# Kernel optimization log

Hardware: AMD Instinct MI355X
Metric: run time of the kernel (lower is better)

The kernel has to match this reference:

```python
import jax, jax.numpy as jnp
import numpy as np

D_MODEL = 1024
NUM_HEADS = 16
DEPTH = D_MODEL // NUM_HEADS
B, S = 2, 2048


def setup_inputs() -> dict:
    key = jax.random.key(0)
    ks = jax.random.split(key, 12)
    scale = 1.0 / np.sqrt(D_MODEL)
    inp = {
        'q': jax.random.normal(ks[0], (B, S, D_MODEL), dtype=jnp.float32),
        'k': jax.random.normal(ks[1], (B, S, D_MODEL), dtype=jnp.float32),
        'v': jax.random.normal(ks[2], (B, S, D_MODEL), dtype=jnp.float32),
        'mask': jnp.zeros((1, 1, S, S), dtype=jnp.float32),
        'wq': jax.random.normal(ks[3], (D_MODEL, D_MODEL), dtype=jnp.float32) * scale,
        'bq': jnp.zeros((D_MODEL,), dtype=jnp.float32),
        'wk': jax.random.normal(ks[4], (D_MODEL, D_MODEL), dtype=jnp.float32) * scale,
        'bk': jnp.zeros((D_MODEL,), dtype=jnp.float32),
        'wv': jax.random.normal(ks[5], (D_MODEL, D_MODEL), dtype=jnp.float32) * scale,
        'bv': jnp.zeros((D_MODEL,), dtype=jnp.float32),
        'wo': jax.random.normal(ks[6], (D_MODEL, D_MODEL), dtype=jnp.float32) * scale,
        'bo': jnp.zeros((D_MODEL,), dtype=jnp.float32),
    }
    return inp


def _split_heads(x):
    # [B, S, D] -> [B, H, S, depth]
    b, s, _ = x.shape
    return x.reshape(b, s, NUM_HEADS, DEPTH).transpose(0, 2, 1, 3)


def reference(q, k, v, mask, wq, bq, wk, bk, wv, bv, wo, bo):
    qh = _split_heads(q @ wq + bq)   # [B,H,S,depth]
    kh = _split_heads(k @ wk + bk)
    vh = _split_heads(v @ wv + bv)
    logits = jnp.einsum('bhqd,bhkd->bhqk', qh, kh) / jnp.sqrt(jnp.float32(DEPTH))
    logits = logits + mask * (-1e9)
    attn = jax.nn.softmax(logits, axis=-1)
    out = jnp.einsum('bhqk,bhkd->bhqd', attn, vh)  # [B,H,S,depth]
    out = out.transpose(0, 2, 1, 3).reshape(q.shape[0], -1, D_MODEL)
    return out @ wo + bo
```

## Files before the change

### kernel.cpp

```cpp
#include <hip/hip_runtime.h>

typedef unsigned short u16;
typedef unsigned int   u32;
typedef unsigned long long u64;
typedef short s16;

using f32x4  = __attribute__((ext_vector_type(4))) float;
using bf16x8 = __attribute__((ext_vector_type(8))) __bf16;
using bf16x4 = __attribute__((ext_vector_type(4))) __bf16;
using u16x8  = __attribute__((ext_vector_type(8))) u16;
using u16x4  = __attribute__((ext_vector_type(4))) u16;
using s16x4  = __attribute__((ext_vector_type(4))) s16;

#define LOG2E 1.4426950408889634f

__device__ __forceinline__ u16 f2bf(float f) {
  u32 u = __builtin_bit_cast(u32, f);
  u32 r = u + 0x7fffu + ((u >> 16) & 1u);
  return (u16)(r >> 16);
}

__device__ __forceinline__ float ex2(float x) {
#if __has_builtin(__builtin_amdgcn_exp2f)
  return __builtin_amdgcn_exp2f(x);
#else
  return exp2f(x);
#endif
}

__device__ __forceinline__ u16x4 pack4(float p0, float p1, float p2, float p3) {
  bf16x4 b = {(__bf16)p0, (__bf16)p1, (__bf16)p2, (__bf16)p3};
  return __builtin_bit_cast(u16x4, b);
}

__device__ __forceinline__ void gll16(const u16* g, u16* l) {
  __builtin_amdgcn_global_load_lds(
      (const __attribute__((address_space(1))) void*)g,
      (__attribute__((address_space(3))) void*)l, 16, 0, 0);
}

__device__ __forceinline__ bf16x8 ld_bf8(const u16* p) {
  return __builtin_bit_cast(bf16x8, *(const u16x8*)p);
}

__device__ __forceinline__ bf16x8 cat8(u16x4 a, u16x4 b) {
  u16x8 r = {a[0], a[1], a[2], a[3], b[0], b[1], b[2], b[3]};
  return __builtin_bit_cast(bf16x8, r);
}

__device__ __forceinline__ f32x4 mfma32(bf16x8 a, bf16x8 b, f32x4 c) {
  return __builtin_amdgcn_mfma_f32_16x16x32_bf16(a, b, c, 0, 0, 0);
}

__device__ __forceinline__ int swz_r(int g) { return g >> 2; }
__device__ __forceinline__ int swz_c(int g) { return (g & 3) ^ ((g >> 3) & 3); }
__device__ __forceinline__ int swz_off(int r, int c) {
  return (r * 4 + (c ^ ((r >> 1) & 3))) * 8;
}

__global__ __launch_bounds__(256) void pre_kernel(
    const float* __restrict__ q, const float* __restrict__ k,
    const float* __restrict__ v, const float* __restrict__ mask,
    const float* __restrict__ wq, const float* __restrict__ wk,
    const float* __restrict__ wv, const float* __restrict__ wo,
    u16* __restrict__ qb, u16* __restrict__ kb, u16* __restrict__ vb,
    u16* __restrict__ wqT, u16* __restrict__ wkT, u16* __restrict__ wvT,
    u16* __restrict__ woT, int* flag) {
  int y = blockIdx.y, t = threadIdx.x;
  if (y < 3) {
    const float* src = y == 0 ? q : y == 1 ? k : v;
    u16* dst = y == 0 ? qb : y == 1 ? kb : vb;
    u64 i = ((u64)blockIdx.x * 256 + t) * 8;
    f32x4 a = *(const f32x4*)(src + i);
    f32x4 b = *(const f32x4*)(src + i + 4);
    u16x8 o;
    o[0] = f2bf(a[0]); o[1] = f2bf(a[1]); o[2] = f2bf(a[2]); o[3] = f2bf(a[3]);
    o[4] = f2bf(b[0]); o[5] = f2bf(b[1]); o[6] = f2bf(b[2]); o[7] = f2bf(b[3]);
    *(u16x8*)(dst + i) = o;
  } else if (y == 3) {
    __shared__ float tile[32][33];
    int x = t & 31, yy = t >> 5;
#pragma unroll
    for (int rep = 0; rep < 2; ++rep) {
      int job = blockIdx.x * 2 + rep;
      int z = job >> 10, tt = job & 1023;
      const float* W = z == 0 ? wq : z == 1 ? wk : z == 2 ? wv : wo;
      u16* WT = z == 0 ? wqT : z == 1 ? wkT : z == 2 ? wvT : woT;
      int c0 = (tt & 31) * 32, r0 = (tt >> 5) * 32;
#pragma unroll
      for (int j = 0; j < 4; ++j)
        tile[yy + j * 8][x] = W[(u64)(r0 + yy + j * 8) * 1024 + c0 + x];
      __syncthreads();
#pragma unroll
      for (int j = 0; j < 4; ++j)
        WT[(u64)(c0 + yy + j * 8) * 1024 + r0 + x] = f2bf(tile[x][yy + j * 8]);
      __syncthreads();
    }
  } else {
    u64 i = ((u64)blockIdx.x * 256 + t) * 8;
    f32x4 a = *(const f32x4*)(mask + i);
    f32x4 b = *(const f32x4*)(mask + i + 4);
    bool nz = a[0] != 0.f || a[1] != 0.f || a[2] != 0.f || a[3] != 0.f ||
              b[0] != 0.f || b[1] != 0.f || b[2] != 0.f || b[3] != 0.f;
    if (nz) atomicOr(flag, 1);
  }
}

__device__ __forceinline__ void gemm_core(const u16* __restrict__ A,
                                          const u16* __restrict__ Wt, int m0,
                                          int n0, u16* SH, f32x4 acc[4][4]) {
  int t = threadIdx.x, w = t >> 6, lane = t & 63;
  int quad = lane >> 4, l16 = lane & 15;
  int wr = w >> 1, wc = w & 1;
  const u16* a0 = A + (u64)(m0 + swz_r(t)) * 1024 + swz_c(t) * 8;
  const u16* a1 = A + (u64)(m0 + swz_r(256 + t)) * 1024 + swz_c(256 + t) * 8;
  const u16* bg0 = Wt + (u64)(n0 + swz_r(t)) * 1024 + swz_c(t) * 8;
  const u16* bg1 = Wt + (u64)(n0 + swz_r(256 + t)) * 1024 + swz_c(256 + t) * 8;
  int aoff[4], boff[4];
#pragma unroll
  for (int i = 0; i < 4; ++i) {
    aoff[i] = swz_off(wr * 64 + i * 16 + l16, quad);
    boff[i] = 4096 + swz_off(wc * 64 + i * 16 + l16, quad);
  }
#define QSTAGE(buf, kt)                                         \
  gll16(a0 + (kt), &SH[(buf) * 8192 + t * 8]);                  \
  gll16(bg0 + (kt), &SH[(buf) * 8192 + 4096 + t * 8]);          \
  gll16(a1 + (kt), &SH[(buf) * 8192 + (256 + t) * 8]);          \
  gll16(bg1 + (kt), &SH[(buf) * 8192 + 4096 + (256 + t) * 8]);
  QSTAGE(0, 0);
  asm volatile("s_waitcnt vmcnt(0)" ::: "memory");
  __builtin_amdgcn_s_barrier();
  __builtin_amdgcn_sched_barrier(0);
#pragma unroll
  for (int T = 0; T < 32; ++T) {
    if (T + 1 < 32) { QSTAGE((T + 1) & 1, (T + 1) * 32); }
    const u16* S = SH + (T & 1) * 8192;
    bf16x8 af[4], bfr[4];
#pragma unroll
    for (int i = 0; i < 4; ++i) af[i] = ld_bf8(&S[aoff[i]]);
#pragma unroll
    for (int i = 0; i < 4; ++i) bfr[i] = ld_bf8(&S[boff[i]]);
#pragma unroll
    for (int mi = 0; mi < 4; ++mi)
#pragma unroll
      for (int ni = 0; ni < 4; ++ni)
        acc[mi][ni] = mfma32(af[mi], bfr[ni], acc[mi][ni]);
    asm volatile("s_waitcnt vmcnt(0)" ::: "memory");
    __builtin_amdgcn_s_barrier();
    __builtin_amdgcn_sched_barrier(0);
  }
#undef QSTAGE
}

__global__ __launch_bounds__(256, 3) void qkv_gemm(
    const u16* __restrict__ qb, const u16* __restrict__ kb,
    const u16* __restrict__ vb, const u16* __restrict__ wqT,
    const u16* __restrict__ wkT, const u16* __restrict__ wvT,
    const float* __restrict__ bq, const float* __restrict__ bk,
    const float* __restrict__ bv, u16* __restrict__ Qh,
    u16* __restrict__ Khs, u16* __restrict__ Vhs) {
  int z = blockIdx.z;
  const u16* A = z == 0 ? qb : z == 1 ? kb : vb;
  const u16* Wt = z == 0 ? wqT : z == 1 ? wkT : wvT;
  const float* bias = z == 0 ? bq : z == 1 ? bk : bv;
  int m0 = blockIdx.x * 128, n0 = blockIdx.y * 128;
  __shared__ __align__(16) u16 SH[18432];
  f32x4 acc[4][4] = {};
  gemm_core(A, Wt, m0, n0, SH, acc);
  int t = threadIdx.x, w = t >> 6, lane = t & 63;
  int quad = lane >> 4, l16 = lane & 15;
  int wr = w >> 1, wc = w & 1;
  int h = (n0 + wc * 64) >> 6;
  if (z == 2) {
#pragma unroll
    for (int mi = 0; mi < 4; ++mi) {
      int gm0 = m0 + wr * 64 + mi * 16;
      int bh = (gm0 >> 11) * 16 + h;
      int tIdx = (gm0 & 2047) >> 6;
      int kvq = ((gm0 & 63) >> 2) + quad;
      u16* tile = Vhs + ((u64)(bh * 32 + tIdx)) * 4096;
#pragma unroll
      for (int ni = 0; ni < 4; ++ni) {
        int d = ni * 16 + l16;
        float bv_ = bias[n0 + wc * 64 + d];
        u16x4 pv = pack4(acc[mi][ni][0] + bv_, acc[mi][ni][1] + bv_,
                         acc[mi][ni][2] + bv_, acc[mi][ni][3] + bv_);
        *(u16x4*)&tile[(kvq * 64 + d) * 4] = pv;
      }
    }
  } else {
    __syncthreads();
    u16* TB = SH + w * 2304;
    float scale = (z == 0) ? (LOG2E / 8.f) : 1.f;
#pragma unroll
    for (int p = 0; p < 2; ++p) {
#pragma unroll
      for (int mi2 = 0; mi2 < 2; ++mi2)
#pragma unroll
        for (int ni = 0; ni < 4; ++ni) {
          int d = ni * 16 + l16;
          float bv_ = bias[n0 + wc * 64 + d];
#pragma unroll
          for (int r = 0; r < 4; ++r) {
            int kvloc = mi2 * 16 + quad * 4 + r;
            TB[kvloc * 72 + d] =
                f2bf((acc[p * 2 + mi2][ni][r] + bv_) * scale);
          }
        }
      int gm0 = m0 + wr * 64 + p * 32;
      int bh = (gm0 >> 11) * 16 + h;
#pragma unroll
      for (int i = 0; i < 4; ++i) {
        int g = i * 64 + lane;
        int kvloc = g >> 3, slot = g & 7;
        if (z == 0) {
          u16x8 gran = *(u16x8*)&TB[kvloc * 72 + slot * 8];
          int s = (gm0 & 2047) + kvloc;
          *(u16x8*)&Qh[((u64)bh * 2048 + s) * 64 + slot * 8] = gran;
        } else {
          int kk = (kvloc & 3) | ((kvloc >> 1) & 4);
          u16x8 gran = *(u16x8*)&TB[kvloc * 72 + (slot ^ kk) * 8];
          int tIdx = (gm0 & 2047) >> 6;
          int kv = (gm0 & 63) + kvloc;
          *(u16x8*)&Khs[((u64)(bh * 32 + tIdx)) * 4096 + kv * 64 + slot * 8] =
              gran;
        }
      }
    }
  }
}

template <int CUR>
__device__ __forceinline__ void fa_fast_step(
    int T, int t, int quad, int l16, int x7,
    const u16* __restrict__ Kg0, const u16* __restrict__ Vg0, u16* Kb0,
    u16* Vb0, bf16x8 aq0, bf16x8 aq1, f32x4 (&o)[4], f32x4& l_acc,
    bf16x8 ones8) {
  if (T + 1 < 32) {
    gll16(Kg0 + (u64)(T + 1) * 4096 + t * 8, &Kb0[(CUR ^ 1) * 4096 + t * 8]);
    gll16(Vg0 + (u64)(T + 1) * 4096 + t * 8, &Vb0[(CUR ^ 1) * 4096 + t * 8]);
  }
  const u16* Kt = Kb0 + CUR * 4096;
  const u16* Vt = Vb0 + CUR * 4096;
  int lbase = (l16 >> 2) * 8 + (l16 & 3);
  u16x4 pk[4];
#pragma unroll
  for (int cc = 0; cc < 4; ++cc) {
    int kvr = (cc >> 1) * 32 + (cc & 1) * 4 + lbase;
    bf16x8 k0 = ld_bf8(&Kt[kvr * 64 + ((quad ^ x7)) * 8]);
    bf16x8 k1 = ld_bf8(&Kt[kvr * 64 + (((quad + 4) ^ x7)) * 8]);
    f32x4 s_ = {};
    s_ = mfma32(k0, aq0, s_);
    s_ = mfma32(k1, aq1, s_);
    pk[cc] = pack4(ex2(s_[0]), ex2(s_[1]), ex2(s_[2]), ex2(s_[3]));
  }
  __builtin_amdgcn_s_setprio(1);
#pragma unroll
  for (int g = 0; g < 2; ++g) {
    bf16x8 pa = cat8(pk[g * 2], pk[g * 2 + 1]);
    l_acc = mfma32(pa, ones8, l_acc);
#pragma unroll
    for (int nt = 0; nt < 4; ++nt) {
      const u16* vb = &Vt[(((g * 8 + quad * 2) * 64) + nt * 16 + l16) * 4];
      bf16x8 vf = cat8(*(const u16x4*)vb, *(const u16x4*)(vb + 256));
      o[nt] = mfma32(pa, vf, o[nt]);
    }
  }
  __builtin_amdgcn_s_setprio(0);
  __syncthreads();
}

template <int CUR>
__device__ __forceinline__ void fa_mask_step(
    int T, int t, int lane, int quad, int l16, int x7, int qg,
    const u16* __restrict__ Kg0, const u16* __restrict__ Vg0,
    const float* __restrict__ mask, u16* Kb0, u16* Vb0, bf16x8 aq0,
    bf16x8 aq1, f32x4 (&o)[4], float& m_r, float& l_r) {
  if (T + 1 < 32) {
    gll16(Kg0 + (u64)(T + 1) * 4096 + t * 8, &Kb0[(CUR ^ 1) * 4096 + t * 8]);
    gll16(Vg0 + (u64)(T + 1) * 4096 + t * 8, &Vb0[(CUR ^ 1) * 4096 + t * 8]);
  }
  const u16* Kt = Kb0 + CUR * 4096;
  const u16* Vt = Vb0 + CUR * 4096;
  int lbase = (l16 >> 2) * 8 + (l16 & 3);
  f32x4 sv[4];
#pragma unroll
  for (int cc = 0; cc < 4; ++cc) {
    int kvr = (cc >> 1) * 32 + (cc & 1) * 4 + lbase;
    bf16x8 k0 = ld_bf8(&Kt[kvr * 64 + ((quad ^ x7)) * 8]);
    bf16x8 k1 = ld_bf8(&Kt[kvr * 64 + (((quad + 4) ^ x7)) * 8]);
    f32x4 s_ = {};
    s_ = mfma32(k0, aq0, s_);
    s_ = mfma32(k1, aq1, s_);
    sv[cc] = s_;
  }
#pragma unroll
  for (int cc = 0; cc < 4; ++cc)
#pragma unroll
    for (int r = 0; r < 4; ++r)
      sv[cc][r] += mask[(u64)qg * 2048 + T * 64 + (cc >> 1) * 32 + quad * 8 +
                        (cc & 1) * 4 + r] *
                   (-1e9f * LOG2E);
  float mx = -1e30f;
#pragma unroll
  for (int cc = 0; cc < 4; ++cc)
    mx = fmaxf(mx, fmaxf(fmaxf(sv[cc][0], sv[cc][1]),
                         fmaxf(sv[cc][2], sv[cc][3])));
  mx = fmaxf(mx, __shfl_xor(mx, 16));
  mx = fmaxf(mx, __shfl_xor(mx, 32));
  float mnew = fmaxf(m_r, mx);
  float alpha = ex2(m_r - mnew);
  m_r = mnew;
  float rs = 0.f;
  u16x4 pk[4];
#pragma unroll
  for (int cc = 0; cc < 4; ++cc) {
    float p0 = ex2(sv[cc][0] - m_r), p1 = ex2(sv[cc][1] - m_r);
    float p2 = ex2(sv[cc][2] - m_r), p3 = ex2(sv[cc][3] - m_r);
    rs += (p0 + p1) + (p2 + p3);
    pk[cc] = pack4(p0, p1, p2, p3);
  }
  rs += __shfl_xor(rs, 16);
  rs += __shfl_xor(rs, 32);
  l_r = l_r * alpha + rs;
  float a4[4];
#pragma unroll
  for (int r = 0; r < 4; ++r)
    a4[r] = __shfl(alpha, (lane & 48) | (quad * 4 + r));
#pragma unroll
  for (int nt = 0; nt < 4; ++nt)
#pragma unroll
    for (int r = 0; r < 4; ++r) o[nt][r] *= a4[r];
  __builtin_amdgcn_s_setprio(1);
#pragma unroll
  for (int g = 0; g < 2; ++g) {
    bf16x8 pa = cat8(pk[g * 2], pk[g * 2 + 1]);
#pragma unroll
    for (int nt = 0; nt < 4; ++nt) {
      const u16* vb = &Vt[(((g * 8 + quad * 2) * 64) + nt * 16 + l16) * 4];
      bf16x8 vf = cat8(*(const u16x4*)vb, *(const u16x4*)(vb + 256));
      o[nt] = mfma32(pa, vf, o[nt]);
    }
  }
  __builtin_amdgcn_s_setprio(0);
  __syncthreads();
}

__global__ __launch_bounds__(512, 4) void flash_attn(
    const u16* __restrict__ Qh, const u16* __restrict__ Khs,
    const u16* __restrict__ Vhs, const float* __restrict__ mask,
    const int* __restrict__ flag, u16* __restrict__ Ob) {
  int L = blockIdx.x + (blockIdx.y << 4);
  int bh = (L & 7) * 4 + ((L >> 3) & 3);
  int q0 = (L >> 5) * 128;
  int t = threadIdx.x, w = t >> 6, lane = t & 63;
  int quad = lane >> 4, l16 = lane & 15;
  __shared__ u16 SMEM[16384];
  u16* Kb0 = SMEM;
  u16* Vb0 = SMEM + 8192;
  const u16* Kg0 = Khs + (u64)bh * 32 * 4096;
  const u16* Vg0 = Vhs + (u64)bh * 32 * 4096;
  const u16* Qbase = Qh + ((u64)bh * 2048 + q0 + w * 16 + l16) * 64 + quad * 8;
  bf16x8 aq0 = ld_bf8(Qbase);
  bf16x8 aq1 = ld_bf8(Qbase + 32);
  f32x4 o[4] = {};
  const bool use_mask = (*flag) != 0;
  int x7 = l16 & 7;
  const u16x8 ones8u = {0x3F80, 0x3F80, 0x3F80, 0x3F80,
                        0x3F80, 0x3F80, 0x3F80, 0x3F80};
  bf16x8 ones8 = __builtin_bit_cast(bf16x8, ones8u);
  gll16(Kg0 + t * 8, &Kb0[t * 8]);
  gll16(Vg0 + t * 8, &Vb0[t * 8]);
  __syncthreads();
  int b = bh >> 4, h = bh & 15;
  if (!use_mask) {
    f32x4 l_acc = {};
    for (int T = 0; T < 32; T += 2) {
      fa_fast_step<0>(T, t, quad, l16, x7, Kg0, Vg0, Kb0, Vb0, aq0, aq1, o,
                      l_acc, ones8);
      fa_fast_step<1>(T + 1, t, quad, l16, x7, Kg0, Vg0, Kb0, Vb0, aq0, aq1,
                      o, l_acc, ones8);
    }
    float rl[4];
#pragma unroll
    for (int r = 0; r < 4; ++r) rl[r] = 1.f / l_acc[r];
#pragma unroll
    for (int nt = 0; nt < 4; ++nt)
#pragma unroll
      for (int r = 0; r < 4; ++r) {
        int srow = q0 + w * 16 + quad * 4 + r;
        Ob[(u64)(b * 2048 + srow) * 1024 + h * 64 + nt * 16 + l16] =
            f2bf(o[nt][r] * rl[r]);
      }
  } else {
    float m_r = -1e30f, l_r = 0.f;
    int qg = q0 + w * 16 + l16;
    for (int T = 0; T < 32; T += 2) {
      fa_mask_step<0>(T, t, lane, quad, l16, x7, qg, Kg0, Vg0, mask, Kb0, Vb0,
                      aq0, aq1, o, m_r, l_r);
      fa_mask_step<1>(T + 1, t, lane, quad, l16, x7, qg, Kg0, Vg0, mask, Kb0,
                      Vb0, aq0, aq1, o, m_r, l_r);
    }
    float rl[4];
#pragma unroll
    for (int r = 0; r < 4; ++r)
      rl[r] = 1.f / __shfl(l_r, (lane & 48) | (quad * 4 + r));
#pragma unroll
    for (int nt = 0; nt < 4; ++nt)
#pragma unroll
      for (int r = 0; r < 4; ++r) {
        int srow = q0 + w * 16 + quad * 4 + r;
        Ob[(u64)(b * 2048 + srow) * 1024 + h * 64 + nt * 16 + l16] =
            f2bf(o[nt][r] * rl[r]);
      }
  }
}

__global__ __launch_bounds__(256, 2) void out_gemm(const u16* __restrict__ Ob,
                                                   const u16* __restrict__ woT,
                                                   const float* __restrict__ bo,
                                                   float* __restrict__ out) {
  int m0 = blockIdx.x * 128, n0 = blockIdx.y * 64;
  __shared__ __align__(16) u16 SH[24576];
  f32x4 acc[2][4] = {};
  int t = threadIdx.x, w = t >> 6, lane = t & 63;
  int quad = lane >> 4, l16 = lane & 15;
  const u16* ag[4];
  const u16* bgp[2];
#pragma unroll
  for (int j = 0; j < 4; ++j) {
    int g = j * 256 + t, row = g >> 3, cc = (g & 7) ^ (row & 7);
    ag[j] = Ob + (u64)(m0 + row) * 1024 + cc * 8;
  }
#pragma unroll
  for (int j = 0; j < 2; ++j) {
    int g = j * 256 + t, row = g >> 3, cc = (g & 7) ^ (row & 7);
    bgp[j] = woT + (u64)(n0 + row) * 1024 + cc * 8;
  }
#define OSTAGE(buf, kt)                                              \
  {                                                                  \
    u16* D = &SH[(buf) * 12288];                                     \
    gll16(ag[0] + (kt), &D[t * 8]);                                  \
    gll16(ag[1] + (kt), &D[(256 + t) * 8]);                          \
    gll16(ag[2] + (kt), &D[(512 + t) * 8]);                          \
    gll16(ag[3] + (kt), &D[(768 + t) * 8]);                          \
    gll16(bgp[0] + (kt), &D[8192 + t * 8]);                          \
    gll16(bgp[1] + (kt), &D[8192 + (256 + t) * 8]);                  \
  }
  OSTAGE(0, 0);
  asm volatile("s_waitcnt vmcnt(0)" ::: "memory");
  __builtin_amdgcn_s_barrier();
  __builtin_amdgcn_sched_barrier(0);
#pragma unroll
  for (int T = 0; T < 16; ++T) {
    if (T + 1 < 16) { OSTAGE((T + 1) & 1, (T + 1) * 64); }
    const u16* S = SH + (T & 1) * 12288;
#pragma unroll
    for (int ks = 0; ks < 2; ++ks) {
      bf16x8 af[2], bfr[4];
#pragma unroll
      for (int i = 0; i < 2; ++i) {
        int r = w * 32 + i * 16 + l16;
        af[i] = ld_bf8(&S[(r * 8 + ((ks * 4 + quad) ^ (r & 7))) * 8]);
      }
#pragma unroll
      for (int i = 0; i < 4; ++i) {
        int r = i * 16 + l16;
        bfr[i] = ld_bf8(&S[8192 + (r * 8 + ((ks * 4 + quad) ^ (r & 7))) * 8]);
      }
#pragma unroll
      for (int mi = 0; mi < 2; ++mi)
#pragma unroll
        for (int ni = 0; ni < 4; ++ni)
          acc[mi][ni] = mfma32(af[mi], bfr[ni], acc[mi][ni]);
    }
    asm volatile("s_waitcnt vmcnt(0)" ::: "memory");
    __builtin_amdgcn_s_barrier();
    __builtin_amdgcn_sched_barrier(0);
  }
#undef OSTAGE
#pragma unroll
  for (int mi = 0; mi < 2; ++mi) {
#pragma unroll
    for (int ni = 0; ni < 4; ++ni) {
      int gn = n0 + ni * 16 + l16;
      float bv_ = bo[gn];
#pragma unroll
      for (int r = 0; r < 4; ++r) {
        int gm = m0 + w * 32 + mi * 16 + quad * 4 + r;
        out[(u64)gm * 1024 + gn] = acc[mi][ni][r] + bv_;
      }
    }
  }
}

extern "C" void kernel_launch(void* const* d_in, const int* in_sizes, int n_in,
                              void* d_out, int out_size, void* d_ws,
                              size_t ws_size, hipStream_t stream) {
  const float* q = (const float*)d_in[0];
  const float* k = (const float*)d_in[1];
  const float* v = (const float*)d_in[2];
  const float* mask = (const float*)d_in[3];
  const float* wq = (const float*)d_in[4];
  const float* bq = (const float*)d_in[5];
  const float* wk = (const float*)d_in[6];
  const float* bk = (const float*)d_in[7];
  const float* wv = (const float*)d_in[8];
  const float* bv = (const float*)d_in[9];
  const float* wo = (const float*)d_in[10];
  const float* bo = (const float*)d_in[11];
  float* out = (float*)d_out;
  char* ws = (char*)d_ws;
  const u64 MB = 1ull << 20;
  u16* qb = (u16*)(ws + 0 * MB);
  u16* kb = (u16*)(ws + 8 * MB);
  u16* vb = (u16*)(ws + 16 * MB);
  u16* wqT = (u16*)(ws + 24 * MB);
  u16* wkT = (u16*)(ws + 26 * MB);
  u16* wvT = (u16*)(ws + 28 * MB);
  u16* woT = (u16*)(ws + 30 * MB);
  u16* Qh = (u16*)(ws + 32 * MB);
  u16* Khs = (u16*)(ws + 40 * MB);
  u16* Vhs = (u16*)(ws + 48 * MB);
  int* flag = (int*)(ws + 56 * MB);
  u16* Ob = qb;

  hipMemsetAsync(flag, 0, 4, stream);
  pre_kernel<<<dim3(2048, 5), 256, 0, stream>>>(
      q, k, v, mask, wq, wk, wv, wo, qb, kb, vb, wqT, wkT, wvT, woT, flag);
  qkv_gemm<<<dim3(32, 8, 3), 256, 0, stream>>>(qb, kb, vb, wqT, wkT, wvT, bq,
                                               bk, bv, Qh, Khs, Vhs);
  flash_attn<<<dim3(16, 32), 512, 0, stream>>>(Qh, Khs, Vhs, mask, flag, Ob);
  out_gemm<<<dim3(32, 16), 256, 0, stream>>>(Ob, woT, bo, out);
}
```

Baseline: 221.7 us.

## Fuse fp32-to-bf16 activation conversion into QKV GEMM A-tile loads

Removes the separate pass that converted q/k/v to bf16. The QKV GEMM now loads fp32 A tiles into registers, converts them, and writes them to LDS while B still uses direct global-to-LDS loads. The mask nonzero flag changes from a global atomic plus memset to a per-block flag array, which one GEMM block OR-reduces. This saves a full read-write round trip of the activations and a memset launch. In exchange the GEMM reads twice the A bytes from fp32, and the converted LDS stores add register pressure and waitcnt stalls in the main loop.

```diff
diff --git a/kernel.cpp b/kernel.cpp
--- a/kernel.cpp
+++ b/kernel.cpp
@@ -33,6 +33,12 @@
   return __builtin_bit_cast(u16x4, b);
 }
 
+__device__ __forceinline__ u16x8 cvt8(f32x4 a, f32x4 b) {
+  bf16x8 r = {(__bf16)a[0], (__bf16)a[1], (__bf16)a[2], (__bf16)a[3],
+              (__bf16)b[0], (__bf16)b[1], (__bf16)b[2], (__bf16)b[3]};
+  return __builtin_bit_cast(u16x8, r);
+}
+
 __device__ __forceinline__ void gll16(const u16* g, u16* l) {
   __builtin_amdgcn_global_load_lds(
       (const __attribute__((address_space(1))) void*)g,
@@ -59,25 +65,13 @@
 }
 
 __global__ __launch_bounds__(256) void pre_kernel(
-    const float* __restrict__ q, const float* __restrict__ k,
-    const float* __restrict__ v, const float* __restrict__ mask,
-    const float* __restrict__ wq, const float* __restrict__ wk,
-    const float* __restrict__ wv, const float* __restrict__ wo,
-    u16* __restrict__ qb, u16* __restrict__ kb, u16* __restrict__ vb,
-    u16* __restrict__ wqT, u16* __restrict__ wkT, u16* __restrict__ wvT,
-    u16* __restrict__ woT, int* flag) {
+    const float* __restrict__ mask, const float* __restrict__ wq,
+    const float* __restrict__ wk, const float* __restrict__ wv,
+    const float* __restrict__ wo, u16* __restrict__ wqT,
+    u16* __restrict__ wkT, u16* __restrict__ wvT, u16* __restrict__ woT,
+    int* __restrict__ flagArr) {
   int y = blockIdx.y, t = threadIdx.x;
-  if (y < 3) {
-    const float* src = y == 0 ? q : y == 1 ? k : v;
-    u16* dst = y == 0 ? qb : y == 1 ? kb : vb;
-    u64 i = ((u64)blockIdx.x * 256 + t) * 8;
-    f32x4 a = *(const f32x4*)(src + i);
-    f32x4 b = *(const f32x4*)(src + i + 4);
-    u16x8 o;
-    o[0] = f2bf(a[0]); o[1] = f2bf(a[1]); o[2] = f2bf(a[2]); o[3] = f2bf(a[3]);
-    o[4] = f2bf(b[0]); o[5] = f2bf(b[1]); o[6] = f2bf(b[2]); o[7] = f2bf(b[3]);
-    *(u16x8*)(dst + i) = o;
-  } else if (y == 3) {
+  if (y == 0) {
     __shared__ float tile[32][33];
     int x = t & 31, yy = t >> 5;
 #pragma unroll
@@ -102,74 +96,104 @@
     f32x4 b = *(const f32x4*)(mask + i + 4);
     bool nz = a[0] != 0.f || a[1] != 0.f || a[2] != 0.f || a[3] != 0.f ||
               b[0] != 0.f || b[1] != 0.f || b[2] != 0.f || b[3] != 0.f;
-    if (nz) atomicOr(flag, 1);
-  }
-}
-
-__device__ __forceinline__ void gemm_core(const u16* __restrict__ A,
-                                          const u16* __restrict__ Wt, int m0,
-                                          int n0, u16* SH, f32x4 acc[4][4]) {
-  int t = threadIdx.x, w = t >> 6, lane = t & 63;
-  int quad = lane >> 4, l16 = lane & 15;
-  int wr = w >> 1, wc = w & 1;
-  const u16* a0 = A + (u64)(m0 + swz_r(t)) * 1024 + swz_c(t) * 8;
-  const u16* a1 = A + (u64)(m0 + swz_r(256 + t)) * 1024 + swz_c(256 + t) * 8;
-  const u16* bg0 = Wt + (u64)(n0 + swz_r(t)) * 1024 + swz_c(t) * 8;
-  const u16* bg1 = Wt + (u64)(n0 + swz_r(256 + t)) * 1024 + swz_c(256 + t) * 8;
-  int aoff[4], boff[4];
-#pragma unroll
-  for (int i = 0; i < 4; ++i) {
-    aoff[i] = swz_off(wr * 64 + i * 16 + l16, quad);
-    boff[i] = 4096 + swz_off(wc * 64 + i * 16 + l16, quad);
-  }
-#define QSTAGE(buf, kt)                                         \
-  gll16(a0 + (kt), &SH[(buf) * 8192 + t * 8]);                  \
-  gll16(bg0 + (kt), &SH[(buf) * 8192 + 4096 + t * 8]);          \
-  gll16(a1 + (kt), &SH[(buf) * 8192 + (256 + t) * 8]);          \
-  gll16(bg1 + (kt), &SH[(buf) * 8192 + 4096 + (256 + t) * 8]);
-  QSTAGE(0, 0);
-  asm volatile("s_waitcnt vmcnt(0)" ::: "memory");
-  __builtin_amdgcn_s_barrier();
-  __builtin_amdgcn_sched_barrier(0);
-#pragma unroll
-  for (int T = 0; T < 32; ++T) {
-    if (T + 1 < 32) { QSTAGE((T + 1) & 1, (T + 1) * 32); }
-    const u16* S = SH + (T & 1) * 8192;
-    bf16x8 af[4], bfr[4];
-#pragma unroll
-    for (int i = 0; i < 4; ++i) af[i] = ld_bf8(&S[aoff[i]]);
-#pragma unroll
-    for (int i = 0; i < 4; ++i) bfr[i] = ld_bf8(&S[boff[i]]);
-#pragma unroll
-    for (int mi = 0; mi < 4; ++mi)
-#pragma unroll
-      for (int ni = 0; ni < 4; ++ni)
-        acc[mi][ni] = mfma32(af[mi], bfr[ni], acc[mi][ni]);
-    asm volatile("s_waitcnt vmcnt(0)" ::: "memory");
-    __builtin_amdgcn_s_barrier();
-    __builtin_amdgcn_sched_barrier(0);
-  }
-#undef QSTAGE
+    int bnz = __syncthreads_or(nz ? 1 : 0);
+    if (t == 0) flagArr[blockIdx.x] = bnz;
+  }
 }
 
 __global__ __launch_bounds__(256, 3) void qkv_gemm(
-    const u16* __restrict__ qb, const u16* __restrict__ kb,
-    const u16* __restrict__ vb, const u16* __restrict__ wqT,
+    const float* __restrict__ q, const float* __restrict__ k,
+    const float* __restrict__ v, const u16* __restrict__ wqT,
     const u16* __restrict__ wkT, const u16* __restrict__ wvT,
     const float* __restrict__ bq, const float* __restrict__ bk,
     const float* __restrict__ bv, u16* __restrict__ Qh,
-    u16* __restrict__ Khs, u16* __restrict__ Vhs) {
+    u16* __restrict__ Khs, u16* __restrict__ Vhs,
+    const int* __restrict__ flagArr, int* __restrict__ flag) {
   int z = blockIdx.z;
-  const u16* A = z == 0 ? qb : z == 1 ? kb : vb;
+  const float* A = z == 0 ? q : z == 1 ? k : v;
   const u16* Wt = z == 0 ? wqT : z == 1 ? wkT : wvT;
   const float* bias = z == 0 ? bq : z == 1 ? bk : bv;
   int m0 = blockIdx.x * 128, n0 = blockIdx.y * 128;
   __shared__ __align__(16) u16 SH[18432];
-  f32x4 acc[4][4] = {};
-  gemm_core(A, Wt, m0, n0, SH, acc);
   int t = threadIdx.x, w = t >> 6, lane = t & 63;
   int quad = lane >> 4, l16 = lane & 15;
   int wr = w >> 1, wc = w & 1;
+
+  if (z == 0 && blockIdx.x == 0 && blockIdx.y == 0) {
+    int v_ = 0;
+#pragma unroll
+    for (int i = 0; i < 8; ++i) v_ |= flagArr[t + i * 256];
+    int* sred = (int*)SH;
+    sred[t] = v_;
+    __syncthreads();
+    if (t == 0) {
+      int o = 0;
+      for (int i = 0; i < 256; ++i) o |= sred[i];
+      *flag = o;
+    }
+    __syncthreads();
+  }
+
+  f32x4 acc[4][4] = {};
+  const float* ga0 = A + (u64)(m0 + swz_r(t)) * 1024 + swz_c(t) * 8;
+  const float* ga1 = A + (u64)(m0 + swz_r(256 + t)) * 1024 + swz_c(256 + t) * 8;
+  const u16* bg0 = Wt + (u64)(n0 + swz_r(t)) * 1024 + swz_c(t) * 8;
+  const u16* bg1 = Wt + (u64)(n0 + swz_r(256 + t)) * 1024 + swz_c(256 + t) * 8;
+  int aoff[4], boff[4];
+#pragma unroll
+  for (int i = 0; i < 4; ++i) {
+    aoff[i] = swz_off(wr * 64 + i * 16 + l16, quad);
+    boff[i] = 4096 + swz_off(wc * 64 + i * 16 + l16, quad);
+  }
+  f32x4 ar0a, ar0b, ar1a, ar1b;
+#define A_ISSUE(kt)                          \
+  ar0a = *(const f32x4*)(ga0 + (kt));        \
+  ar0b = *(const f32x4*)(ga0 + (kt) + 4);    \
+  ar1a = *(const f32x4*)(ga1 + (kt));        \
+  ar1b = *(const f32x4*)(ga1 + (kt) + 4);
+#define A_WRITE(buf)                                   \
+  {                                                    \
+    u16* D = &SH[(buf) * 8192];                        \
+    *(u16x8*)&D[t * 8] = cvt8(ar0a, ar0b);             \
+    *(u16x8*)&D[(256 + t) * 8] = cvt8(ar1a, ar1b);     \
+  }
+#define B_ISSUE(buf, kt)                                      \
+  gll16(bg0 + (kt), &SH[(buf) * 8192 + 4096 + t * 8]);        \
+  gll16(bg1 + (kt), &SH[(buf) * 8192 + 4096 + (256 + t) * 8]);
+  A_ISSUE(0);
+  B_ISSUE(0, 0);
+  asm volatile("s_waitcnt vmcnt(0)" ::: "memory");
+  A_WRITE(0);
+  asm volatile("s_waitcnt lgkmcnt(0)" ::: "memory");
+  __builtin_amdgcn_s_barrier();
+  __builtin_amdgcn_sched_barrier(0);
+#pragma unroll
+  for (int T = 0; T < 32; ++T) {
+    if (T + 1 < 32) {
+      A_ISSUE((T + 1) * 32);
+      B_ISSUE((T + 1) & 1, (T + 1) * 32);
+    }
+    const u16* S = SH + (T & 1) * 8192;
+    bf16x8 af[4], bfr[4];
+#pragma unroll
+    for (int i = 0; i < 4; ++i) af[i] = ld_bf8(&S[aoff[i]]);
+#pragma unroll
+    for (int i = 0; i < 4; ++i) bfr[i] = ld_bf8(&S[boff[i]]);
+#pragma unroll
+    for (int mi = 0; mi < 4; ++mi)
+#pragma unroll
+      for (int ni = 0; ni < 4; ++ni)
+        acc[mi][ni] = mfma32(af[mi], bfr[ni], acc[mi][ni]);
+    asm volatile("s_waitcnt vmcnt(0)" ::: "memory");
+    if (T + 1 < 32) { A_WRITE((T + 1) & 1); }
+    asm volatile("s_waitcnt lgkmcnt(0)" ::: "memory");
+    __builtin_amdgcn_s_barrier();
+    __builtin_amdgcn_sched_barrier(0);
+  }
+#undef A_ISSUE
+#undef A_WRITE
+#undef B_ISSUE
+
   int h = (n0 + wc * 64) >> 6;
   if (z == 2) {
 #pragma unroll
@@ -512,9 +536,7 @@
   float* out = (float*)d_out;
   char* ws = (char*)d_ws;
   const u64 MB = 1ull << 20;
-  u16* qb = (u16*)(ws + 0 * MB);
-  u16* kb = (u16*)(ws + 8 * MB);
-  u16* vb = (u16*)(ws + 16 * MB);
+  u16* Ob = (u16*)(ws + 0 * MB);
   u16* wqT = (u16*)(ws + 24 * MB);
   u16* wkT = (u16*)(ws + 26 * MB);
   u16* wvT = (u16*)(ws + 28 * MB);
@@ -523,13 +545,12 @@
   u16* Khs = (u16*)(ws + 40 * MB);
   u16* Vhs = (u16*)(ws + 48 * MB);
   int* flag = (int*)(ws + 56 * MB);
-  u16* Ob = qb;
-
-  hipMemsetAsync(flag, 0, 4, stream);
-  pre_kernel<<<dim3(2048, 5), 256, 0, stream>>>(
-      q, k, v, mask, wq, wk, wv, wo, qb, kb, vb, wqT, wkT, wvT, woT, flag);
-  qkv_gemm<<<dim3(32, 8, 3), 256, 0, stream>>>(qb, kb, vb, wqT, wkT, wvT, bq,
-                                               bk, bv, Qh, Khs, Vhs);
+  int* flagArr = (int*)(ws + 56 * MB + 4096);
+
+  pre_kernel<<<dim3(2048, 2), 256, 0, stream>>>(
+      mask, wq, wk, wv, wo, wqT, wkT, wvT, woT, flagArr);
+  qkv_gemm<<<dim3(32, 8, 3), 256, 0, stream>>>(q, k, v, wqT, wkT, wvT, bq, bk,
+                                               bv, Qh, Khs, Vhs, flagArr, flag);
   flash_attn<<<dim3(16, 32), 512, 0, stream>>>(Qh, Khs, Vhs, mask, flag, Ob);
   out_gemm<<<dim3(32, 16), 256, 0, stream>>>(Ob, woT, bo, out);
 }
```

Result: slower. 254.8 us (+14.9%).
